# Optimization experiments

Measured on AMD Instinct MI355X. Metric: run time of the kernel, lower is better.

## Reference

```python
import jax, jax.numpy as jnp
import numpy as np

B, N, C, H, W = 16, 10, 128, 48, 48

def setup_inputs() -> dict:
    key = jax.random.key(0)
    k0, k1 = jax.random.split(key, 2)
    x = jax.random.normal(k0, (B, N, C, H, W), dtype=jnp.float32)
    # trainable interpolation params, initialized to 0.5 as in the torch module
    pos_dec = jnp.full((N,), 0.5, dtype=jnp.float32)
    length_dec = jnp.full((N,), 0.5, dtype=jnp.float32)
    # 1x1 conv == channel-mixing matmul over N*C channels
    NC = N * C
    conv_w = jax.random.normal(k1, (NC, NC), dtype=jnp.float32) * (1.0 / np.sqrt(NC))
    conv_b = jnp.zeros((NC,), dtype=jnp.float32)
    return {"x": x, "pos_dec": pos_dec, "length_dec": length_dec,
            "conv_w": conv_w, "conv_b": conv_b}


def reference(x, pos_dec, length_dec, conv_w, conv_b):
    b, n, c, h, w = x.shape
    d = c * h * w
    q = x.reshape(b, n, d)          # proj_query (B,N,CHW)
    k = q                           # proj_key has the same flattened features
    # bi_interpolate with pos_int=i, length_int=1 reduces in closed form to:
    #   s0 = (1-pd)*K[i]   + pd*K[i+1]                      (key_short row)
    #   s1 = ld*((1-pd)*K[i+1] + pd*K[i+2])                 (zero-padded short mixed with key_long)
    # where indices wrap mod N (key was concatenated with itself).
    idx = jnp.arange(n)
    k1_ = k[:, (idx + 1) % n]       # (B,N,D)
    k2_ = k[:, (idx + 2) % n]
    pd = pos_dec[None, :, None]
    ld = length_dec[None, :, None]
    s0 = (1.0 - pd) * k + pd * k1_
    s1 = ld * ((1.0 - pd) * k1_ + pd * k2_)
    S = jnp.stack([s0, s1], axis=2)                 # (B,N,2,D) interpolated keys per group
    logits = jnp.einsum('bnd,bnkd->bnk', q, S)      # per-group 2-way attention scores
    attn = jax.nn.softmax(logits, axis=-1)          # softmax over the 2 searched keys
    out = jnp.einsum('bnk,bnkd->bnd', attn, S)      # (B,N,D)
    feat = out.reshape(b, n * c, h, w)
    conv = jnp.einsum('oc,bchw->bohw', conv_w, feat) + conv_b[None, :, None, None]
    return conv + x.reshape(b, n * c, h, w)
```

## Files before the change

kernel.cpp:

```cpp
#include <hip/hip_runtime.h>
#include <hip/hip_bf16.h>

#define BB 16
#define NN 10
#define CC 128
#define HWD 2304
#define DD (CC*HWD)
#define NC (NN*CC)
#define CHK 36
#define CHUNK (DD/CHK)

#define BM 256
#define BN 256
#define BK2 32
#define NHALF (NC/BK2)

typedef __bf16 bf16x8 __attribute__((ext_vector_type(8)));
typedef float  f32x4  __attribute__((ext_vector_type(4)));

#define FEAT_BYTES ((size_t)BB*HWD*NC*2)
#define WB_BYTES   ((size_t)NC*NC*2)
#define PART_FLOATS (BB*NN*CHK*3)

__device__ __forceinline__ ushort f2bf(float f) {
    __hip_bfloat16 h = __float2bfloat16(f);
    return *reinterpret_cast<ushort*>(&h);
}

__device__ __forceinline__ void gload_lds16(const ushort* g, ushort* l) {
    __builtin_amdgcn_global_load_lds(
        (const __attribute__((address_space(1))) void*)(const void*)g,
        (__attribute__((address_space(3))) void*)(void*)l,
        16, 0, 0);
}

__global__ __launch_bounds__(256) void k_dots(const float* __restrict__ x,
                                              float* __restrict__ part) {
    int blk = blockIdx.x;
    int bn = blk / CHK, ch = blk % CHK;
    int b = bn / NN, n = bn % NN;
    int n1 = (n + 1) % NN, n2 = (n + 2) % NN;
    const float* p0 = x + ((size_t)b*NN + n )*DD + (size_t)ch*CHUNK;
    const float* p1 = x + ((size_t)b*NN + n1)*DD + (size_t)ch*CHUNK;
    const float* p2 = x + ((size_t)b*NN + n2)*DD + (size_t)ch*CHUNK;
    int t = threadIdx.x;
    float s0 = 0.f, s1 = 0.f, s2 = 0.f;
    #pragma unroll
    for (int i = 0; i < CHUNK/1024; ++i) {
        int off = i*1024 + t*4;
        float4 a = *(const float4*)(p0 + off);
        float4 u = *(const float4*)(p1 + off);
        float4 v = *(const float4*)(p2 + off);
        s0 += a.x*a.x + a.y*a.y + a.z*a.z + a.w*a.w;
        s1 += a.x*u.x + a.y*u.y + a.z*u.z + a.w*u.w;
        s2 += a.x*v.x + a.y*v.y + a.z*v.z + a.w*v.w;
    }
    for (int o = 32; o > 0; o >>= 1) {
        s0 += __shfl_down(s0, o);
        s1 += __shfl_down(s1, o);
        s2 += __shfl_down(s2, o);
    }
    __shared__ float red[4][3];
    int w = t >> 6, l = t & 63;
    if (l == 0) { red[w][0] = s0; red[w][1] = s1; red[w][2] = s2; }
    __syncthreads();
    if (t == 0) {
        float r0 = 0.f, r1 = 0.f, r2 = 0.f;
        for (int i = 0; i < 4; ++i) { r0 += red[i][0]; r1 += red[i][1]; r2 += red[i][2]; }
        float* o = part + ((size_t)bn*CHK + ch)*3;
        o[0] = r0; o[1] = r1; o[2] = r2;
    }
}

__global__ void k_coef(const float* __restrict__ part,
                       const float* __restrict__ pos_dec,
                       const float* __restrict__ len_dec,
                       float* __restrict__ coef) {
    int bn = threadIdx.x;
    if (bn >= BB*NN) return;
    int n = bn % NN;
    float d0 = 0.f, d1 = 0.f, d2 = 0.f;
    const float* p = part + (size_t)bn*CHK*3;
    for (int i = 0; i < CHK; ++i) { d0 += p[i*3]; d1 += p[i*3+1]; d2 += p[i*3+2]; }
    float pd = pos_dec[n], ld = len_dec[n];
    float l0 = (1.f - pd)*d0 + pd*d1;
    float l1 = ld*((1.f - pd)*d1 + pd*d2);
    float m  = fmaxf(l0, l1);
    float e0 = expf(l0 - m), e1 = expf(l1 - m);
    float inv = 1.f/(e0 + e1);
    float a0 = e0*inv, a1 = e1*inv;
    coef[bn*3+0] = a0*(1.f - pd);
    coef[bn*3+1] = a0*pd + a1*ld*(1.f - pd);
    coef[bn*3+2] = a1*ld*pd;
}

__global__ __launch_bounds__(256) void k_wconv(const float* __restrict__ w,
                                               ushort* __restrict__ wb) {
    int i = blockIdx.x*blockDim.x + threadIdx.x;
    size_t idx = (size_t)i*4;
    if (idx >= (size_t)NC*NC) return;
    float4 a = *(const float4*)(w + idx);
    ushort4 o;
    o.x = f2bf(a.x); o.y = f2bf(a.y); o.z = f2bf(a.z); o.w = f2bf(a.w);
    *(ushort4*)(wb + idx) = o;
}

__global__ __launch_bounds__(256) void k_feat(const float* __restrict__ x,
                                              const float* __restrict__ coef,
                                              ushort* __restrict__ featT) {
    __shared__ float tile[32*129];
    int hwt = blockIdx.x;
    int n   = blockIdx.y;
    int b   = blockIdx.z;
    int bn  = b*NN + n;
    float c0 = coef[bn*3+0], c1 = coef[bn*3+1], c2 = coef[bn*3+2];
    int n1 = (n + 1) % NN, n2 = (n + 2) % NN;
    const float* p0 = x + ((size_t)b*NN + n )*DD;
    const float* p1 = x + ((size_t)b*NN + n1)*DD;
    const float* p2 = x + ((size_t)b*NN + n2)*DD;
    int t = threadIdx.x;
    int hw0 = hwt*32;

    int ccl = t >> 3;
    int hwi = (t & 7) * 4;
    #pragma unroll
    for (int p = 0; p < 4; ++p) {
        int cc = p*32 + ccl;
        size_t off = (size_t)cc*HWD + hw0 + hwi;
        float4 a = *(const float4*)(p0 + off);
        float4 u = *(const float4*)(p1 + off);
        float4 v = *(const float4*)(p2 + off);
        tile[(hwi+0)*129 + cc] = c0*a.x + c1*u.x + c2*v.x;
        tile[(hwi+1)*129 + cc] = c0*a.y + c1*u.y + c2*v.y;
        tile[(hwi+2)*129 + cc] = c0*a.z + c1*u.z + c2*v.z;
        tile[(hwi+3)*129 + cc] = c0*a.w + c1*u.w + c2*v.w;
    }
    __syncthreads();

    int hwl = t >> 4;
    int cc0 = (t & 15) * 8;
    #pragma unroll
    for (int p = 0; p < 2; ++p) {
        int hw = p*16 + hwl;
        const float* src = &tile[hw*129 + cc0];
        union { ushort us[8]; uint4 v; } pk;
        #pragma unroll
        for (int j = 0; j < 8; ++j) pk.us[j] = f2bf(src[j]);
        ushort* dst = featT + (size_t)b*HWD*NC + (size_t)(hw0 + hw)*NC + n*CC + cc0;
        *(uint4*)dst = pk.v;
    }
}

__global__ __launch_bounds__(512, 2) void k_gemm(const ushort* __restrict__ Wb,
                                                 const ushort* __restrict__ featT,
                                                 const float* __restrict__ bias,
                                                 const float* __restrict__ x,
                                                 float* __restrict__ out) {
    __shared__ ushort S[4][2][BM*BK2];

    int bid = blockIdx.x;
    int wkid = (bid & 7) * 90 + (bid >> 3);
    int b   = wkid / 45;
    int r45 = wkid % 45;
    int hwt = r45 / 5;
    int ot  = r45 % 5;
    int o0 = ot*BM, hw0 = hwt*BN;

    int t = threadIdx.x;
    int l = t & 63;
    int w = t >> 6;
    int wr = w >> 2, wc = w & 3;

    const ushort* Ag = Wb + (size_t)o0*NC;
    const ushort* Bg = featT + (size_t)b*HWD*NC + (size_t)hw0*NC;

    int sl0 = t, sl1 = 512 + t;
    int sr0 = sl0 >> 2, sc0 = sl0 & 3;
    int sr1 = sl1 >> 2, sc1 = sl1 & 3;
    size_t ga0 = (size_t)sr0*NC + (size_t)((sc0 ^ ((sr0 >> 1) & 3)) * 8);
    size_t ga1 = (size_t)sr1*NC + (size_t)((sc1 ^ ((sr1 >> 1) & 3)) * 8);

#define STAGE_A(ht_) do { ushort* d_ = &S[(ht_)&3][0][0]; size_t ko_ = (size_t)(ht_)*BK2; \
    gload_lds16(Ag + ga0 + ko_, d_ + sl0*8); \
    gload_lds16(Ag + ga1 + ko_, d_ + sl1*8); } while(0)
#define STAGE_B(ht_) do { ushort* d_ = &S[(ht_)&3][1][0]; size_t ko_ = (size_t)(ht_)*BK2; \
    gload_lds16(Bg + ga0 + ko_, d_ + sl0*8); \
    gload_lds16(Bg + ga1 + ko_, d_ + sl1*8); } while(0)

    int rowA0 = wr*128 + (l & 15);
    int rowB0 = wc*64  + (l & 15);
    int ksw   = ((l >> 4) ^ ((l >> 1) & 3)) * 8;

    f32x4 acc[8][4] = {};

    STAGE_A(0); STAGE_B(0);
    STAGE_A(1); STAGE_B(1);
    STAGE_A(2); STAGE_B(2);
    asm volatile("s_waitcnt vmcnt(8)" ::: "memory");
    __builtin_amdgcn_s_barrier();
    __builtin_amdgcn_sched_barrier(0);

    for (int ht = 0; ht < NHALF; ++ht) {
        const ushort* as = &S[ht & 3][0][0];
        const ushort* bs = &S[ht & 3][1][0];

        bf16x8 bfr[4], af0[4], af1[4];
        #pragma unroll
        for (int n = 0; n < 4; ++n)
            bfr[n] = *(const bf16x8*)&bs[(rowB0 + n*16)*BK2 + ksw];
        #pragma unroll
        for (int i = 0; i < 4; ++i)
            af0[i] = *(const bf16x8*)&as[(rowA0 + i*16)*BK2 + ksw];
        if (ht + 3 < NHALF) STAGE_A(ht + 3);
        __builtin_amdgcn_s_barrier();
        __builtin_amdgcn_sched_barrier(0);
        __builtin_amdgcn_s_setprio(1);
        #pragma unroll
        for (int i = 0; i < 4; ++i)
            #pragma unroll
            for (int n = 0; n < 4; ++n)
                acc[i][n] = __builtin_amdgcn_mfma_f32_16x16x32_bf16(af0[i], bfr[n], acc[i][n], 0, 0, 0);
        __builtin_amdgcn_s_setprio(0);
        __builtin_amdgcn_s_barrier();
        __builtin_amdgcn_sched_barrier(0);

        #pragma unroll
        for (int i = 0; i < 4; ++i)
            af1[i] = *(const bf16x8*)&as[(rowA0 + 64 + i*16)*BK2 + ksw];
        if (ht + 3 < NHALF) STAGE_B(ht + 3);
        if (ht < NHALF - 3)       asm volatile("s_waitcnt vmcnt(8)" ::: "memory");
        else if (ht == NHALF - 3) asm volatile("s_waitcnt vmcnt(4)" ::: "memory");
        else if (ht == NHALF - 2) asm volatile("s_waitcnt vmcnt(0)" ::: "memory");
        __builtin_amdgcn_s_barrier();
        __builtin_amdgcn_sched_barrier(0);
        __builtin_amdgcn_s_setprio(1);
        #pragma unroll
        for (int i = 0; i < 4; ++i)
            #pragma unroll
            for (int n = 0; n < 4; ++n)
                acc[4+i][n] = __builtin_amdgcn_mfma_f32_16x16x32_bf16(af1[i], bfr[n], acc[4+i][n], 0, 0, 0);
        __builtin_amdgcn_s_setprio(0);
        __builtin_amdgcn_s_barrier();
        __builtin_amdgcn_sched_barrier(0);
    }
#undef STAGE_A
#undef STAGE_B

    #pragma unroll
    for (int m = 0; m < 8; ++m) {
        int ro_base = o0 + wr*128 + m*16 + ((l >> 4) << 2);
        #pragma unroll
        for (int n = 0; n < 4; ++n) {
            int col = hw0 + wc*64 + n*16 + (l & 15);
            #pragma unroll
            for (int r = 0; r < 4; ++r) {
                int ro = ro_base + r;
                size_t idx = (size_t)b*NC*HWD + (size_t)ro*HWD + col;
                out[idx] = acc[m][n][r] + bias[ro] + x[idx];
            }
        }
    }
}

extern "C" void kernel_launch(void* const* d_in, const int* in_sizes, int n_in,
                              void* d_out, int out_size, void* d_ws, size_t ws_size,
                              hipStream_t stream) {
    const float* x       = (const float*)d_in[0];
    const float* pos_dec = (const float*)d_in[1];
    const float* len_dec = (const float*)d_in[2];
    const float* conv_w  = (const float*)d_in[3];
    const float* conv_b  = (const float*)d_in[4];
    float* out = (float*)d_out;

    char* ws = (char*)d_ws;
    ushort* featT = (ushort*)ws;
    ushort* wb    = (ushort*)(ws + FEAT_BYTES);
    float*  part  = (float*)(ws + FEAT_BYTES + WB_BYTES);
    float*  coef  = part + PART_FLOATS;

    k_dots <<<dim3(BB*NN*CHK), 256, 0, stream>>>(x, part);
    k_coef <<<dim3(1), 256, 0, stream>>>(part, pos_dec, len_dec, coef);
    k_wconv<<<dim3(1600), 256, 0, stream>>>(conv_w, wb);
    k_feat <<<dim3(72, NN, BB), 256, 0, stream>>>(x, coef, featT);
    k_gemm <<<dim3(720), 512, 0, stream>>>(wb, featT, conv_b, x, out);
}
```

Before: 305.8 us.

## Restructure GEMM pipeline to double-buffered BK=64 with four sub-stages

The GEMM main loop changes from a 4-deep ring of BK=32 half-tiles to a double-buffered BK=64 tile split into four 32-wide regions. Each region is staged and waited on separately, interleaved with MFMA phases, and the LDS swizzle and load mapping are rewritten to match. The k_dots block index is also reordered so that consecutive blocks walk over n, which changes L2 locality among the overlapping x rows. The intent is a different balance of prefetch depth and barrier count, at the cost of a shallower prefetch distance.

```diff
diff --git a/kernel.cpp b/kernel.cpp
--- a/kernel.cpp
+++ b/kernel.cpp
@@ -12,8 +12,8 @@
 
 #define BM 256
 #define BN 256
-#define BK2 32
-#define NHALF (NC/BK2)
+#define BK 64
+#define TK (NC/BK)
 
 typedef __bf16 bf16x8 __attribute__((ext_vector_type(8)));
 typedef float  f32x4  __attribute__((ext_vector_type(4)));
@@ -37,8 +37,11 @@
 __global__ __launch_bounds__(256) void k_dots(const float* __restrict__ x,
                                               float* __restrict__ part) {
     int blk = blockIdx.x;
-    int bn = blk / CHK, ch = blk % CHK;
-    int b = bn / NN, n = bn % NN;
+    int n  = blk % NN;
+    int rest = blk / NN;
+    int ch = rest % CHK;
+    int b  = rest / CHK;
+    int bn = b*NN + n;
     int n1 = (n + 1) % NN, n2 = (n + 2) % NN;
     const float* p0 = x + ((size_t)b*NN + n )*DD + (size_t)ch*CHUNK;
     const float* p1 = x + ((size_t)b*NN + n1)*DD + (size_t)ch*CHUNK;
@@ -156,7 +159,7 @@
                                                  const float* __restrict__ bias,
                                                  const float* __restrict__ x,
                                                  float* __restrict__ out) {
-    __shared__ ushort S[4][2][BM*BK2];
+    __shared__ ushort L[2][4][BM*32];
 
     int bid = blockIdx.x;
     int wkid = (bid & 7) * 90 + (bid >> 3);
@@ -174,44 +177,50 @@
     const ushort* Ag = Wb + (size_t)o0*NC;
     const ushort* Bg = featT + (size_t)b*HWD*NC + (size_t)hw0*NC;
 
-    int sl0 = t, sl1 = 512 + t;
-    int sr0 = sl0 >> 2, sc0 = sl0 & 3;
-    int sr1 = sl1 >> 2, sc1 = sl1 & 3;
-    size_t ga0 = (size_t)sr0*NC + (size_t)((sc0 ^ ((sr0 >> 1) & 3)) * 8);
-    size_t ga1 = (size_t)sr1*NC + (size_t)((sc1 ^ ((sr1 >> 1) & 3)) * 8);
-
-#define STAGE_A(ht_) do { ushort* d_ = &S[(ht_)&3][0][0]; size_t ko_ = (size_t)(ht_)*BK2; \
-    gload_lds16(Ag + ga0 + ko_, d_ + sl0*8); \
-    gload_lds16(Ag + ga1 + ko_, d_ + sl1*8); } while(0)
-#define STAGE_B(ht_) do { ushort* d_ = &S[(ht_)&3][1][0]; size_t ko_ = (size_t)(ht_)*BK2; \
-    gload_lds16(Bg + ga0 + ko_, d_ + sl0*8); \
-    gload_lds16(Bg + ga1 + ko_, d_ + sl1*8); } while(0)
-
-    int rowA0 = wr*128 + (l & 15);
-    int rowB0 = wc*64  + (l & 15);
-    int ksw   = ((l >> 4) ^ ((l >> 1) & 3)) * 8;
+    int r0 = t >> 2, c0 = t & 3;
+    int r1 = r0 + 128, c1 = c0;
+    int sw = (t >> 3) & 3;
+    size_t g0 = (size_t)r0*NC + (size_t)((c0 ^ sw) * 8);
+    size_t g1 = (size_t)r1*NC + (size_t)((c1 ^ sw) * 8);
+
+#define STAGE(gbase_, nb_, reg_, tile_, q_) do { \
+    ushort* d_ = &L[nb_][reg_][0]; \
+    size_t ko_ = (size_t)(tile_)*BK + (q_)*32; \
+    gload_lds16((gbase_) + g0 + ko_, d_ + t*8); \
+    gload_lds16((gbase_) + g1 + ko_, d_ + (512 + t)*8); } while (0)
+
+    int fr = l & 15;
+    int fsw = (l >> 1) & 3;
+    int kc = ((l >> 4) ^ fsw) * 8;
+    int rowA0 = wr*128 + fr;
+    int rowB0 = wc*64 + fr;
 
     f32x4 acc[8][4] = {};
 
-    STAGE_A(0); STAGE_B(0);
-    STAGE_A(1); STAGE_B(1);
-    STAGE_A(2); STAGE_B(2);
-    asm volatile("s_waitcnt vmcnt(8)" ::: "memory");
+    STAGE(Ag, 0, 0, 0, 0); STAGE(Bg, 0, 1, 0, 0);
+    STAGE(Ag, 0, 2, 0, 1); STAGE(Bg, 0, 3, 0, 1);
+    asm volatile("s_waitcnt vmcnt(4)" ::: "memory");
     __builtin_amdgcn_s_barrier();
     __builtin_amdgcn_sched_barrier(0);
 
-    for (int ht = 0; ht < NHALF; ++ht) {
-        const ushort* as = &S[ht & 3][0][0];
-        const ushort* bs = &S[ht & 3][1][0];
-
-        bf16x8 bfr[4], af0[4], af1[4];
+    bf16x8 b0f[4], b1f[4], af[4];
+
+    for (int kt = 0; kt < TK; ++kt) {
+        int buf = kt & 1, nbuf = buf ^ 1;
+        const ushort* A0r = &L[buf][0][0];
+        const ushort* B0r = &L[buf][1][0];
+        const ushort* A1r = &L[buf][2][0];
+        const ushort* B1r = &L[buf][3][0];
+        bool more = (kt + 1 < TK);
+
         #pragma unroll
         for (int n = 0; n < 4; ++n)
-            bfr[n] = *(const bf16x8*)&bs[(rowB0 + n*16)*BK2 + ksw];
-        #pragma unroll
-        for (int i = 0; i < 4; ++i)
-            af0[i] = *(const bf16x8*)&as[(rowA0 + i*16)*BK2 + ksw];
-        if (ht + 3 < NHALF) STAGE_A(ht + 3);
+            b0f[n] = *(const bf16x8*)&B0r[(rowB0 + n*16)*32 + kc];
+        #pragma unroll
+        for (int i = 0; i < 4; ++i)
+            af[i] = *(const bf16x8*)&A0r[(rowA0 + i*16)*32 + kc];
+        if (more) STAGE(Ag, nbuf, 0, kt+1, 0);
+        __builtin_amdgcn_sched_barrier(0);
         __builtin_amdgcn_s_barrier();
         __builtin_amdgcn_sched_barrier(0);
         __builtin_amdgcn_s_setprio(1);
@@ -219,18 +228,17 @@
         for (int i = 0; i < 4; ++i)
             #pragma unroll
             for (int n = 0; n < 4; ++n)
-                acc[i][n] = __builtin_amdgcn_mfma_f32_16x16x32_bf16(af0[i], bfr[n], acc[i][n], 0, 0, 0);
+                acc[i][n] = __builtin_amdgcn_mfma_f32_16x16x32_bf16(af[i], b0f[n], acc[i][n], 0, 0, 0);
         __builtin_amdgcn_s_setprio(0);
-        __builtin_amdgcn_s_barrier();
-        __builtin_amdgcn_sched_barrier(0);
-
-        #pragma unroll
-        for (int i = 0; i < 4; ++i)
-            af1[i] = *(const bf16x8*)&as[(rowA0 + 64 + i*16)*BK2 + ksw];
-        if (ht + 3 < NHALF) STAGE_B(ht + 3);
-        if (ht < NHALF - 3)       asm volatile("s_waitcnt vmcnt(8)" ::: "memory");
-        else if (ht == NHALF - 3) asm volatile("s_waitcnt vmcnt(4)" ::: "memory");
-        else if (ht == NHALF - 2) asm volatile("s_waitcnt vmcnt(0)" ::: "memory");
+        __builtin_amdgcn_sched_barrier(0);
+        __builtin_amdgcn_s_barrier();
+        __builtin_amdgcn_sched_barrier(0);
+
+        #pragma unroll
+        for (int i = 0; i < 4; ++i)
+            af[i] = *(const bf16x8*)&A0r[(rowA0 + 64 + i*16)*32 + kc];
+        if (more) STAGE(Bg, nbuf, 1, kt+1, 0);
+        __builtin_amdgcn_sched_barrier(0);
         __builtin_amdgcn_s_barrier();
         __builtin_amdgcn_sched_barrier(0);
         __builtin_amdgcn_s_setprio(1);
@@ -238,13 +246,55 @@
         for (int i = 0; i < 4; ++i)
             #pragma unroll
             for (int n = 0; n < 4; ++n)
-                acc[4+i][n] = __builtin_amdgcn_mfma_f32_16x16x32_bf16(af1[i], bfr[n], acc[4+i][n], 0, 0, 0);
+                acc[4+i][n] = __builtin_amdgcn_mfma_f32_16x16x32_bf16(af[i], b0f[n], acc[4+i][n], 0, 0, 0);
         __builtin_amdgcn_s_setprio(0);
-        __builtin_amdgcn_s_barrier();
-        __builtin_amdgcn_sched_barrier(0);
-    }
-#undef STAGE_A
-#undef STAGE_B
+        __builtin_amdgcn_sched_barrier(0);
+        if (more) asm volatile("s_waitcnt vmcnt(4)" ::: "memory");
+        else      asm volatile("s_waitcnt vmcnt(0)" ::: "memory");
+        __builtin_amdgcn_s_barrier();
+        __builtin_amdgcn_sched_barrier(0);
+
+        #pragma unroll
+        for (int n = 0; n < 4; ++n)
+            b1f[n] = *(const bf16x8*)&B1r[(rowB0 + n*16)*32 + kc];
+        #pragma unroll
+        for (int i = 0; i < 4; ++i)
+            af[i] = *(const bf16x8*)&A1r[(rowA0 + i*16)*32 + kc];
+        if (more) STAGE(Ag, nbuf, 2, kt+1, 1);
+        __builtin_amdgcn_sched_barrier(0);
+        __builtin_amdgcn_s_barrier();
+        __builtin_amdgcn_sched_barrier(0);
+        __builtin_amdgcn_s_setprio(1);
+        #pragma unroll
+        for (int i = 0; i < 4; ++i)
+            #pragma unroll
+            for (int n = 0; n < 4; ++n)
+                acc[i][n] = __builtin_amdgcn_mfma_f32_16x16x32_bf16(af[i], b1f[n], acc[i][n], 0, 0, 0);
+        __builtin_amdgcn_s_setprio(0);
+        __builtin_amdgcn_sched_barrier(0);
+        __builtin_amdgcn_s_barrier();
+        __builtin_amdgcn_sched_barrier(0);
+
+        #pragma unroll
+        for (int i = 0; i < 4; ++i)
+            af[i] = *(const bf16x8*)&A1r[(rowA0 + 64 + i*16)*32 + kc];
+        if (more) STAGE(Bg, nbuf, 3, kt+1, 1);
+        __builtin_amdgcn_sched_barrier(0);
+        __builtin_amdgcn_s_barrier();
+        __builtin_amdgcn_sched_barrier(0);
+        __builtin_amdgcn_s_setprio(1);
+        #pragma unroll
+        for (int i = 0; i < 4; ++i)
+            #pragma unroll
+            for (int n = 0; n < 4; ++n)
+                acc[4+i][n] = __builtin_amdgcn_mfma_f32_16x16x32_bf16(af[i], b1f[n], acc[4+i][n], 0, 0, 0);
+        __builtin_amdgcn_s_setprio(0);
+        __builtin_amdgcn_sched_barrier(0);
+        if (more) asm volatile("s_waitcnt vmcnt(4)" ::: "memory");
+        __builtin_amdgcn_s_barrier();
+        __builtin_amdgcn_sched_barrier(0);
+    }
+#undef STAGE
 
     #pragma unroll
     for (int m = 0; m < 8; ++m) {
```

Result: slower. 326.8 us (+6.9%).
